# Kernel optimization log

Measured on AMD Instinct MI355X. Metric: run time of the kernel, lower is better.

Reference implementation:

```python
import jax, jax.numpy as jnp
import numpy as np

HIDDEN = 768
NUM_HEADS = 12
HEAD_DIM = HIDDEN // NUM_HEADS
B, S = 4, 2048


def setup_inputs() -> dict:
    key = jax.random.key(0)
    ks = jax.random.split(key, 10)
    scale = 1.0 / np.sqrt(HIDDEN)
    return {
        "hidden_states": jax.random.normal(ks[0], (B, S, HIDDEN), dtype=jnp.float32),
        "attention_mask": jnp.ones((B, S), dtype=jnp.float32),
        "Wq": jax.random.normal(ks[1], (HIDDEN, HIDDEN), dtype=jnp.float32) * scale,
        "bq": jnp.zeros((HIDDEN,), dtype=jnp.float32),
        "Wk": jax.random.normal(ks[2], (HIDDEN, HIDDEN), dtype=jnp.float32) * scale,
        "bk": jnp.zeros((HIDDEN,), dtype=jnp.float32),
        "Wv": jax.random.normal(ks[3], (HIDDEN, HIDDEN), dtype=jnp.float32) * scale,
        "bv": jnp.zeros((HIDDEN,), dtype=jnp.float32),
        "Wo": jax.random.normal(ks[4], (HIDDEN, HIDDEN), dtype=jnp.float32) * scale,
        "bo": jnp.zeros((HIDDEN,), dtype=jnp.float32),
    }


def reference(hidden_states, attention_mask, Wq, bq, Wk, bk, Wv, bv, Wo, bo):
    b, s, _ = hidden_states.shape
    # nn.Linear: x @ W.T + b  (W is [out, in])
    Q = hidden_states @ Wq.T + bq
    K = hidden_states @ Wk.T + bk
    V = hidden_states @ Wv.T + bv
    # [b, s, h*d] -> [b, h, s, d]
    Q = Q.reshape(b, s, NUM_HEADS, HEAD_DIM).transpose(0, 2, 1, 3)
    K = K.reshape(b, s, NUM_HEADS, HEAD_DIM).transpose(0, 2, 1, 3)
    V = V.reshape(b, s, NUM_HEADS, HEAD_DIM).transpose(0, 2, 1, 3)
    # scores: [b, h, s, s]
    scores = jnp.einsum("bhqd,bhkd->bhqk", Q, K) / jnp.sqrt(
        jnp.asarray(HEAD_DIM, dtype=Q.dtype))
    # mask: [b, s] -> additive bias broadcast over heads and query dim
    bias = (1.0 - attention_mask)[:, None, None, :] * -10000.0
    scores = scores + bias
    probs = jax.nn.softmax(scores, axis=-1)  # dropout p=0.0 -> identity
    context = jnp.einsum("bhqk,bhkd->bhqd", probs, V)
    context = context.transpose(0, 2, 1, 3).reshape(b, s, HIDDEN)
    return context @ Wo.T + bo
```

## Files before the change

kernel.cpp:

```cpp
#include <hip/hip_runtime.h>
#include <hip/hip_bf16.h>

#define SEQ   2048
#define NH    12
#define MTOK  8192

typedef __attribute__((ext_vector_type(8))) short short8;
typedef __attribute__((ext_vector_type(4))) short short4v;
typedef __attribute__((ext_vector_type(4))) float f32x4;
typedef __attribute__((ext_vector_type(16))) float f32x16;
typedef __attribute__((ext_vector_type(2))) unsigned uint2v;

__device__ inline short f2bf(float x) {
  __hip_bfloat16 h = __float2bfloat16(x);
  return *(short*)&h;
}

#define GLL(gp, lp) __builtin_amdgcn_global_load_lds( \
    (const __attribute__((address_space(1))) void*)(gp), \
    (__attribute__((address_space(3))) void*)(lp), 16, 0, 0)

#define GLL4(gp, lp) __builtin_amdgcn_global_load_lds( \
    (const __attribute__((address_space(1))) void*)(gp), \
    (__attribute__((address_space(3))) void*)(lp), 4, 0, 0)

#define MFMA(a, b, c) __builtin_amdgcn_mfma_f32_16x16x32_bf16(a, b, c, 0, 0, 0)

#if !defined(__HIP_DEVICE_COMPILE__)
#define MFMA32(a, b, c) (c)
#else
#define MFMA32(a, b, c) __builtin_amdgcn_mfma_f32_32x32x16_bf16(a, b, c, 0, 0, 0)
#endif

#if !defined(__HIP_DEVICE_COMPILE__)
#define EXP2(x) (x)
#elif __has_builtin(__builtin_amdgcn_exp2f)
#define EXP2(x) __builtin_amdgcn_exp2f(x)
#else
#define EXP2(x) __expf((x) * 0.6931471805599453f)
#endif

__device__ inline unsigned pack2bf(float a, float b) {
  unsigned ua = __float_as_uint(a) + 0x8000u;
  unsigned ub = __float_as_uint(b) + 0x8000u;
#if defined(__HIP_DEVICE_COMPILE__) && __has_builtin(__builtin_amdgcn_perm)
  return __builtin_amdgcn_perm(ub, ua, 0x07060302u);
#else
  return (ub & 0xFFFF0000u) | (ua >> 16);
#endif
}

__device__ inline unsigned packtrunc2(float a, float b) {
#if defined(__HIP_DEVICE_COMPILE__) && __has_builtin(__builtin_amdgcn_perm)
  return __builtin_amdgcn_perm(__float_as_uint(b), __float_as_uint(a),
                               0x07060302u);
#else
  return (__float_as_uint(b) & 0xFFFF0000u) | (__float_as_uint(a) >> 16);
#endif
}

__device__ inline uint2v lane32swap(unsigned a, unsigned b) {
#if defined(__HIP_DEVICE_COMPILE__) && __has_builtin(__builtin_amdgcn_permlane32_swap)
  return __builtin_amdgcn_permlane32_swap(a, b, false, false);
#else
  int lane = (int)(threadIdx.x & 63);
  unsigned xa = (unsigned)__shfl((int)a, lane ^ 32, 64);
  unsigned xb = (unsigned)__shfl((int)b, lane ^ 32, 64);
  bool hi = lane >= 32;
  uint2v r;
  r.x = hi ? xb : a;
  r.y = hi ? b : xa;
  return r;
#endif
}

union PackFrag {
  unsigned u[2];
  short4v s;
};

union Frag8 {
  unsigned u[4];
  short8 s;
};

#define QSCALE 0.18033688011112042f
#define MBSCALE -14426.950408889634f

__global__ __launch_bounds__(256) void prep(
    const float* __restrict__ hs, const float* __restrict__ Wq,
    const float* __restrict__ Wk, const float* __restrict__ Wv,
    const float* __restrict__ Wo, const float* __restrict__ mask,
    short* __restrict__ Xb, short* __restrict__ Wqkvb,
    short* __restrict__ Wob, float* __restrict__ mbias) {
  int bid = blockIdx.x;
  if (bid < 6144) {
    int i = bid * 256 + threadIdx.x;
    float4 v = ((const float4*)hs)[i];
    short4v o;
    o[0] = f2bf(v.x); o[1] = f2bf(v.y); o[2] = f2bf(v.z); o[3] = f2bf(v.w);
    ((short4v*)Xb)[i] = o;
  } else if (bid < 6144 + 2304) {
    int idx = (bid - 6144) * 256 + threadIdx.x;
    int r = idx / 192, c = (idx - r * 192) * 4;
    const float* src;
    short* dst;
    int rr;
    if (r < 768)       { src = Wq; rr = r;        dst = Wqkvb; }
    else if (r < 1536) { src = Wk; rr = r - 768;  dst = Wqkvb; }
    else if (r < 2304) { src = Wv; rr = r - 1536; dst = Wqkvb; }
    else               { src = Wo; rr = r - 2304; dst = Wob; r = rr; }
    float4 v = *(const float4*)&src[(size_t)rr * 768 + c];
    short4v o;
    o[0] = f2bf(v.x); o[1] = f2bf(v.y); o[2] = f2bf(v.z); o[3] = f2bf(v.w);
    *(short4v*)&dst[(size_t)r * 768 + c] = o;
  } else {
    int i = (bid - 6144 - 2304) * 256 + threadIdx.x;
    if (i < MTOK) mbias[i] = (1.f - mask[i]) * MBSCALE;
  }
}

#define GEMM_BK64_LOOP(Aptr, Bptr)                                            \
  __shared__ __align__(16) short As[128 * 64];                                \
  __shared__ __align__(16) short Bs[128 * 64];                                \
  const int t = threadIdx.x;                                                  \
  const int wid = t >> 6, lane = t & 63, l15 = lane & 15, quad = lane >> 4;   \
  const int bm = blockIdx.x * 128, bn = blockIdx.y * 128;                     \
  const int mq = (wid & 1) * 64, nq = (wid >> 1) * 64;                        \
  const int srow8 = lane >> 3;                                                \
  const int schunk = lane & 7;                                                \
  const int scol = (schunk ^ srow8) * 8;                                      \
  f32x4 acc[4][4] = {};                                                       \
  const short *gA[4], *gB[4];                                                 \
  _Pragma("unroll") for (int g = 0; g < 4; ++g) {                             \
    int row = wid * 32 + g * 8 + srow8;                                       \
    gA[g] = (Aptr) + (size_t)(bm + row) * 768 + scol;                         \
    gB[g] = (Bptr) + (size_t)(bn + row) * 768 + scol;                         \
  }                                                                           \
  for (int k0 = 0; k0 < 768; k0 += 64) {                                      \
    _Pragma("unroll") for (int g = 0; g < 4; ++g)                             \
      GLL(gA[g] + k0, &As[(wid * 32 + g * 8) * 64]);                          \
    _Pragma("unroll") for (int g = 0; g < 4; ++g)                             \
      GLL(gB[g] + k0, &Bs[(wid * 32 + g * 8) * 64]);                          \
    __syncthreads();                                                          \
    _Pragma("unroll") for (int ks = 0; ks < 2; ++ks) {                        \
      short8 a[4], b[4];                                                      \
      _Pragma("unroll") for (int mt = 0; mt < 4; ++mt)                        \
        a[mt] = *(const short8*)&As[(mq + mt * 16 + l15) * 64 +               \
                                    (((ks * 4 + quad) ^ (l15 & 7)) * 8)];     \
      _Pragma("unroll") for (int nt = 0; nt < 4; ++nt)                        \
        b[nt] = *(const short8*)&Bs[(nq + nt * 16 + l15) * 64 +               \
                                    (((ks * 4 + quad) ^ (l15 & 7)) * 8)];     \
      _Pragma("unroll") for (int mt = 0; mt < 4; ++mt)                        \
        _Pragma("unroll") for (int nt = 0; nt < 4; ++nt)                      \
          acc[mt][nt] = MFMA(a[mt], b[nt], acc[mt][nt]);                      \
    }                                                                         \
    __syncthreads();                                                          \
  }

__global__ __launch_bounds__(256) void gemm_qkv(
    const short* __restrict__ A, const short* __restrict__ B,
    const float* __restrict__ bq, const float* __restrict__ bk,
    const float* __restrict__ bv, short* __restrict__ Qb,
    short* __restrict__ Kb, short* __restrict__ Vt) {
  GEMM_BK64_LOOP(A, B)

  const int seg = bn >= 1536 ? 2 : (bn >= 768 ? 1 : 0);
  const float* bias = seg == 0 ? bq : (seg == 1 ? bk : bv);
  const int colbase = bn - seg * 768;

  if (seg < 2) {
    short* dst = seg == 0 ? Qb : Kb;
    const float sc = seg == 0 ? QSCALE : 1.f;
#pragma unroll
    for (int mt = 0; mt < 4; ++mt)
#pragma unroll
      for (int nt = 0; nt < 4; ++nt) {
        int col = colbase + nq + nt * 16 + l15;
        float bias_v = bias[col];
#pragma unroll
        for (int i = 0; i < 4; ++i) {
          int row = bm + mq + mt * 16 + quad * 4 + i;
          dst[(size_t)row * 768 + col] = f2bf((acc[mt][nt][i] + bias_v) * sc);
        }
      }
  } else {
#pragma unroll
    for (int mt = 0; mt < 4; ++mt) {
      int row0 = bm + mq + mt * 16 + quad * 4;
      int b_ = row0 >> 11, s = row0 & 2047;
#pragma unroll
      for (int nt = 0; nt < 4; ++nt) {
        int col = colbase + nq + nt * 16 + l15;
        float bias_v = bias[col];
        int h = col >> 6, d = col & 63;
        short4v pv;
#pragma unroll
        for (int i = 0; i < 4; ++i) pv[i] = f2bf(acc[mt][nt][i] + bias_v);
        *(short4v*)&Vt[(((size_t)b_ * NH + h) * 64 + d) * 2048 + s] = pv;
      }
    }
  }
}

__global__ __launch_bounds__(256) void gemm_out(
    const short* __restrict__ A, const short* __restrict__ B,
    const float* __restrict__ bias, float* __restrict__ C) {
  GEMM_BK64_LOOP(A, B)

#pragma unroll
  for (int mt = 0; mt < 4; ++mt)
#pragma unroll
    for (int nt = 0; nt < 4; ++nt) {
      int col = bn + nq + nt * 16 + l15;
      float bias_v = bias[col];
#pragma unroll
      for (int i = 0; i < 4; ++i) {
        int row = bm + mq + mt * 16 + quad * 4 + i;
        C[(size_t)row * 768 + col] = acc[mt][nt][i] + bias_v;
      }
    }
}

__global__ __launch_bounds__(256, 3) void attn_v13(
    const short* __restrict__ Qb, const short* __restrict__ Kb,
    const short* __restrict__ Vt, const float* __restrict__ maskb,
    short* __restrict__ Ctx) {
  __shared__ __align__(16) short Ks[3][64 * 64];
  __shared__ __align__(16) short Vs[3][64 * 64];
  __shared__ __align__(16) float Mbs[3][64];
  const int t = threadIdx.x;
  const int w = t >> 6, lane = t & 63, l31 = lane & 31, hi = lane >> 5;
  const int bh = blockIdx.x, b = bh / NH, h = bh % NH;
  const int q0 = blockIdx.y * 128;

  short8 qb[4];
  {
    int rowq = b * 2048 + q0 + w * 32 + l31;
    const short* qp = &Qb[(size_t)rowq * 768 + h * 64 + hi * 8];
#pragma unroll
    for (int kc = 0; kc < 4; ++kc) qb[kc] = *(const short8*)&qp[kc * 16];
  }

  f32x16 O0 = {}, O1 = {}, lacc = {};
  short8 ones8;
#pragma unroll
  for (int j = 0; j < 8; ++j) ones8[j] = (short)0x3F80;

  const int r0 = w * 16 + (lane >> 3);
  const int pc = lane & 7;
  const int swz0 = (pc ^ (r0 & 7)) * 8;
  const int swz1 = (pc ^ ((r0 + 8) & 7)) * 8;
  const short* gK0 = Kb + (size_t)(b * 2048 + r0) * 768 + h * 64 + swz0;
  const short* gK1 = Kb + (size_t)(b * 2048 + r0 + 8) * 768 + h * 64 + swz1;
  const short* gV0 = Vt + ((size_t)bh * 64 + r0) * 2048 + swz0;
  const short* gV1 = Vt + ((size_t)bh * 64 + r0 + 8) * 2048 + swz1;
  const float* gmb = maskb + b * 2048 + lane;
  const int rs = l31 & 7;

#define STAGE(tt, s) do {                                                     \
    const size_t kn = (size_t)(((tt) & 31) * 64);                             \
    GLL4(gmb + kn, &Mbs[s][0]);                                               \
    GLL(gK0 + kn * 768, &Ks[s][(w * 16) * 64]);                               \
    GLL(gK1 + kn * 768, &Ks[s][(w * 16 + 8) * 64]);                           \
    GLL(gV0 + kn, &Vs[s][(w * 16) * 64]);                                     \
    GLL(gV1 + kn, &Vs[s][(w * 16 + 8) * 64]);                                 \
  } while (0)

#define TILE_SYNC() do {                                                      \
    asm volatile("s_waitcnt vmcnt(5)" ::: "memory");                          \
    __builtin_amdgcn_s_barrier();                                             \
    __builtin_amdgcn_sched_barrier(0);                                        \
  } while (0)

  STAGE(0, 0);
  STAGE(1, 1);
  TILE_SYNC();

  int cur = 0;
  for (int ti = 0; ti < 32; ++ti) {
    const int nx2 = (cur == 0) ? 2 : cur - 1;
    STAGE(ti + 2, nx2);

    short8 pfrag[4];

#pragma unroll
    for (int kb2 = 0; kb2 < 2; ++kb2) {
      f32x16 S;
#pragma unroll
      for (int g = 0; g < 4; ++g) {
        f32x4 m4 = *(const f32x4*)&Mbs[cur][kb2 * 32 + g * 8 + hi * 4];
        S[4 * g + 0] = m4[0]; S[4 * g + 1] = m4[1];
        S[4 * g + 2] = m4[2]; S[4 * g + 3] = m4[3];
      }
#pragma unroll
      for (int kc = 0; kc < 4; ++kc) {
        short8 ka = *(const short8*)&Ks[cur][(kb2 * 32 + l31) * 64 +
                                            (((kc * 2 + hi) ^ rs) * 8)];
        S = MFMA32(ka, qb[kc], S);
      }
      unsigned pk[4][2];
#pragma unroll
      for (int g = 0; g < 4; ++g) {
        float p0 = EXP2(S[4 * g + 0]);
        float p1 = EXP2(S[4 * g + 1]);
        float p2 = EXP2(S[4 * g + 2]);
        float p3 = EXP2(S[4 * g + 3]);
        pk[g][0] = packtrunc2(p0, p1);
        pk[g][1] = packtrunc2(p2, p3);
      }
#pragma unroll
      for (int half = 0; half < 2; ++half) {
        Frag8 f;
        uint2v ra = lane32swap(pk[half * 2][0], pk[half * 2 + 1][0]);
        uint2v rb = lane32swap(pk[half * 2][1], pk[half * 2 + 1][1]);
        f.u[0] = ra.x;
        f.u[1] = rb.x;
        f.u[2] = ra.y;
        f.u[3] = rb.y;
        pfrag[kb2 * 2 + half] = f.s;
      }
    }

#pragma unroll
    for (int c = 0; c < 4; ++c) lacc = MFMA32(ones8, pfrag[c], lacc);

#pragma unroll
    for (int c = 0; c < 4; ++c) {
      short8 av0 = *(const short8*)&Vs[cur][(l31) * 64 +
                                           (((c * 2 + hi) ^ rs) * 8)];
      short8 av1 = *(const short8*)&Vs[cur][(32 + l31) * 64 +
                                           (((c * 2 + hi) ^ rs) * 8)];
      O0 = MFMA32(av0, pfrag[c], O0);
      O1 = MFMA32(av1, pfrag[c], O1);
    }

    TILE_SYNC();
    cur = (cur == 2) ? 0 : cur + 1;
  }

  {
    float inv = 1.f / lacc[0];
    int rowq = b * 2048 + q0 + w * 32 + l31;
    short* cp = &Ctx[(size_t)rowq * 768 + h * 64 + hi * 4];
#pragma unroll
    for (int g = 0; g < 4; ++g) {
      PackFrag pf0, pf1;
      pf0.u[0] = pack2bf(O0[4 * g + 0] * inv, O0[4 * g + 1] * inv);
      pf0.u[1] = pack2bf(O0[4 * g + 2] * inv, O0[4 * g + 3] * inv);
      *(short4v*)&cp[g * 8] = pf0.s;
      pf1.u[0] = pack2bf(O1[4 * g + 0] * inv, O1[4 * g + 1] * inv);
      pf1.u[1] = pack2bf(O1[4 * g + 2] * inv, O1[4 * g + 3] * inv);
      *(short4v*)&cp[32 + g * 8] = pf1.s;
    }
  }
#undef STAGE
#undef TILE_SYNC
}

extern "C" void kernel_launch(void* const* d_in, const int* in_sizes, int n_in,
                              void* d_out, int out_size, void* d_ws,
                              size_t ws_size, hipStream_t stream) {
  const float* hs   = (const float*)d_in[0];
  const float* mask = (const float*)d_in[1];
  const float* Wq   = (const float*)d_in[2];
  const float* bq   = (const float*)d_in[3];
  const float* Wk   = (const float*)d_in[4];
  const float* bk   = (const float*)d_in[5];
  const float* Wv   = (const float*)d_in[6];
  const float* bv   = (const float*)d_in[7];
  const float* Wo   = (const float*)d_in[8];
  const float* bo   = (const float*)d_in[9];

  char* ws = (char*)d_ws;
  short* Xb    = (short*)(ws);
  short* Wqkvb = (short*)(ws + 12582912);
  short* Wob   = (short*)(ws + 16121856);
  short* Qb    = (short*)(ws + 17301504);
  short* Kb    = (short*)(ws + 29884416);
  short* Vtg   = (short*)(ws + 42467328);
  short* Ctxb  = (short*)(ws + 55050240);
  float* mbias = (float*)(ws + 67633152);

  prep<<<8480, 256, 0, stream>>>(hs, Wq, Wk, Wv, Wo, mask,
                                 Xb, Wqkvb, Wob, mbias);
  gemm_qkv<<<dim3(64, 18), 256, 0, stream>>>(Xb, Wqkvb, bq, bk, bv,
                                             Qb, Kb, Vtg);
  attn_v13<<<dim3(48, 16), 256, 0, stream>>>(Qb, Kb, Vtg, mbias, Ctxb);
  gemm_out<<<dim3(64, 6), 256, 0, stream>>>(Ctxb, Wob, bo, (float*)d_out);
}
```

Baseline: 220.8 us.

## Pipeline GEMM K-loop with a three-stage LDS ring buffer

Replaces the single-buffered BK=64 GEMM loop (load, sync, compute, sync) with a BK=32 three-slot ring. Loads run two stages ahead, paced by an explicit vmcnt wait and one barrier per iteration, so global-to-LDS copies overlap the MFMA work. The XOR swizzle is adapted to 32-wide rows. The tail issues redundant wrapped loads (kk%24), which wastes some bandwidth, and correctness depends on the vmcnt counting being right.

```diff
diff --git a/kernel.cpp b/kernel.cpp
--- a/kernel.cpp
+++ b/kernel.cpp
@@ -120,50 +120,62 @@
   }
 }
 
-#define GEMM_BK64_LOOP(Aptr, Bptr)                                            \
-  __shared__ __align__(16) short As[128 * 64];                                \
-  __shared__ __align__(16) short Bs[128 * 64];                                \
+#define GEMM_BK32_RING(Aptr, Bptr)                                            \
+  __shared__ __align__(16) short As[3][128 * 32];                             \
+  __shared__ __align__(16) short Bs[3][128 * 32];                             \
   const int t = threadIdx.x;                                                  \
   const int wid = t >> 6, lane = t & 63, l15 = lane & 15, quad = lane >> 4;   \
   const int bm = blockIdx.x * 128, bn = blockIdx.y * 128;                     \
   const int mq = (wid & 1) * 64, nq = (wid >> 1) * 64;                        \
-  const int srow8 = lane >> 3;                                                \
-  const int schunk = lane & 7;                                                \
-  const int scol = (schunk ^ srow8) * 8;                                      \
+  const int srow = lane >> 2;                                                 \
+  const int schunk = lane & 3;                                                \
   f32x4 acc[4][4] = {};                                                       \
-  const short *gA[4], *gB[4];                                                 \
-  _Pragma("unroll") for (int g = 0; g < 4; ++g) {                             \
-    int row = wid * 32 + g * 8 + srow8;                                       \
+  const short *gA[2], *gB[2];                                                 \
+  _Pragma("unroll") for (int g = 0; g < 2; ++g) {                             \
+    int row = wid * 32 + g * 16 + srow;                                       \
+    int scol = (schunk ^ (row & 3)) * 8;                                      \
     gA[g] = (Aptr) + (size_t)(bm + row) * 768 + scol;                         \
     gB[g] = (Bptr) + (size_t)(bn + row) * 768 + scol;                         \
   }                                                                           \
-  for (int k0 = 0; k0 < 768; k0 += 64) {                                      \
-    _Pragma("unroll") for (int g = 0; g < 4; ++g)                             \
-      GLL(gA[g] + k0, &As[(wid * 32 + g * 8) * 64]);                          \
-    _Pragma("unroll") for (int g = 0; g < 4; ++g)                             \
-      GLL(gB[g] + k0, &Bs[(wid * 32 + g * 8) * 64]);                          \
-    __syncthreads();                                                          \
-    _Pragma("unroll") for (int ks = 0; ks < 2; ++ks) {                        \
-      short8 a[4], b[4];                                                      \
-      _Pragma("unroll") for (int mt = 0; mt < 4; ++mt)                        \
-        a[mt] = *(const short8*)&As[(mq + mt * 16 + l15) * 64 +               \
-                                    (((ks * 4 + quad) ^ (l15 & 7)) * 8)];     \
+  GSTAGE(0, 0);                                                               \
+  GSTAGE(1, 1);                                                               \
+  asm volatile("s_waitcnt vmcnt(4)" ::: "memory");                            \
+  __builtin_amdgcn_s_barrier();                                               \
+  __builtin_amdgcn_sched_barrier(0);                                          \
+  int cur = 0;                                                                \
+  for (int ti = 0; ti < 24; ++ti) {                                           \
+    const int nx2 = (cur == 0) ? 2 : cur - 1;                   \
+    GSTAGE(ti + 2, nx2);                                                      \
+    short8 a[4], b[4];                                                        \
+    _Pragma("unroll") for (int mt = 0; mt < 4; ++mt)                          \
+      a[mt] = *(const short8*)&As[cur][(mq + mt * 16 + l15) * 32 +            \
+                                       ((quad ^ (l15 & 3)) * 8)];             \
+    _Pragma("unroll") for (int nt = 0; nt < 4; ++nt)                          \
+      b[nt] = *(const short8*)&Bs[cur][(nq + nt * 16 + l15) * 32 +            \
+                                       ((quad ^ (l15 & 3)) * 8)];             \
+    _Pragma("unroll") for (int mt = 0; mt < 4; ++mt)                          \
       _Pragma("unroll") for (int nt = 0; nt < 4; ++nt)                        \
-        b[nt] = *(const short8*)&Bs[(nq + nt * 16 + l15) * 64 +               \
-                                    (((ks * 4 + quad) ^ (l15 & 7)) * 8)];     \
-      _Pragma("unroll") for (int mt = 0; mt < 4; ++mt)                        \
-        _Pragma("unroll") for (int nt = 0; nt < 4; ++nt)                      \
-          acc[mt][nt] = MFMA(a[mt], b[nt], acc[mt][nt]);                      \
+        acc[mt][nt] = MFMA(a[mt], b[nt], acc[mt][nt]);                        \
+    asm volatile("s_waitcnt vmcnt(4)" ::: "memory");                          \
+    __builtin_amdgcn_s_barrier();                                             \
+    __builtin_amdgcn_sched_barrier(0);                                        \
+    cur = (cur == 2) ? 0 : cur + 1;                                           \
+  }
+
+#define GSTAGE(kk, s) do {                                                    \
+    const int k0g = ((kk) % 24) * 32;                                         \
+    _Pragma("unroll") for (int g = 0; g < 2; ++g) {                           \
+      GLL(gA[g] + k0g, &As[s][(wid * 32 + g * 16) * 32]);                     \
+      GLL(gB[g] + k0g, &Bs[s][(wid * 32 + g * 16) * 32]);                     \
     }                                                                         \
-    __syncthreads();                                                          \
-  }
+  } while (0)
 
 __global__ __launch_bounds__(256) void gemm_qkv(
     const short* __restrict__ A, const short* __restrict__ B,
     const float* __restrict__ bq, const float* __restrict__ bk,
     const float* __restrict__ bv, short* __restrict__ Qb,
     short* __restrict__ Kb, short* __restrict__ Vt) {
-  GEMM_BK64_LOOP(A, B)
+  GEMM_BK32_RING(A, B)
 
   const int seg = bn >= 1536 ? 2 : (bn >= 768 ? 1 : 0);
   const float* bias = seg == 0 ? bq : (seg == 1 ? bk : bv);
@@ -206,7 +218,7 @@
 __global__ __launch_bounds__(256) void gemm_out(
     const short* __restrict__ A, const short* __restrict__ B,
     const float* __restrict__ bias, float* __restrict__ C) {
-  GEMM_BK64_LOOP(A, B)
+  GEMM_BK32_RING(A, B)
 
 #pragma unroll
   for (int mt = 0; mt < 4; ++mt)
```

New measurement: 239.9 us. 8.6% more time.

## Rewrite projection GEMMs as 8-wave 256x128 double-buffered ping-pong pipeline

Applied to the files above, without the earlier changes.

Replaces the single-buffered 128x128 GEMM loop with a 512-thread, 256x128 tile kernel that double-buffers A/B in LDS. The next k-slice is prefetched via global_load_lds while MFMAs run, using barrier and setprio interleaving between wave groups. This aims to hide global load latency and raise MFMA utilisation in the QKV and output projections. The larger LDS footprint (about 96 KB per block) may limit occupancy, and the grid shrinks to fewer blocks.

```diff
diff --git a/kernel.cpp b/kernel.cpp
--- a/kernel.cpp
+++ b/kernel.cpp
@@ -120,50 +120,76 @@
   }
 }
 
-#define GEMM_BK64_LOOP(Aptr, Bptr)                                            \
-  __shared__ __align__(16) short As[128 * 64];                                \
-  __shared__ __align__(16) short Bs[128 * 64];                                \
+#define GS8(kk, s) do {                                                       \
+    const int k0g = ((kk) % 12) * 64;                                         \
+    _Pragma("unroll") for (int g = 0; g < 4; ++g)                             \
+      GLL(gA[g] + k0g, &As[s][(wid * 32 + g * 8) * 64]);                      \
+    _Pragma("unroll") for (int g = 0; g < 2; ++g)                             \
+      GLL(gB[g] + k0g, &Bs[s][(wid * 16 + g * 8) * 64]);                      \
+  } while (0)
+
+#define GEMM_8P_CORE(Aptr, Bptr)                                              \
+  __shared__ __align__(16) short As[2][256 * 64];                             \
+  __shared__ __align__(16) short Bs[2][128 * 64];                             \
   const int t = threadIdx.x;                                                  \
   const int wid = t >> 6, lane = t & 63, l15 = lane & 15, quad = lane >> 4;   \
-  const int bm = blockIdx.x * 128, bn = blockIdx.y * 128;                     \
-  const int mq = (wid & 1) * 64, nq = (wid >> 1) * 64;                        \
-  const int srow8 = lane >> 3;                                                \
-  const int schunk = lane & 7;                                                \
+  const int bm = blockIdx.x * 256, bn = blockIdx.y * 128;                     \
+  const int wm = wid & 1, wn = wid >> 1;                                      \
+  const int srow8 = lane >> 3, schunk = lane & 7;                             \
   const int scol = (schunk ^ srow8) * 8;                                      \
-  f32x4 acc[4][4] = {};                                                       \
-  const short *gA[4], *gB[4];                                                 \
-  _Pragma("unroll") for (int g = 0; g < 4; ++g) {                             \
-    int row = wid * 32 + g * 8 + srow8;                                       \
-    gA[g] = (Aptr) + (size_t)(bm + row) * 768 + scol;                         \
-    gB[g] = (Bptr) + (size_t)(bn + row) * 768 + scol;                         \
-  }                                                                           \
-  for (int k0 = 0; k0 < 768; k0 += 64) {                                      \
-    _Pragma("unroll") for (int g = 0; g < 4; ++g)                             \
-      GLL(gA[g] + k0, &As[(wid * 32 + g * 8) * 64]);                          \
-    _Pragma("unroll") for (int g = 0; g < 4; ++g)                             \
-      GLL(gB[g] + k0, &Bs[(wid * 32 + g * 8) * 64]);                          \
-    __syncthreads();                                                          \
-    _Pragma("unroll") for (int ks = 0; ks < 2; ++ks) {                        \
-      short8 a[4], b[4];                                                      \
-      _Pragma("unroll") for (int mt = 0; mt < 4; ++mt)                        \
-        a[mt] = *(const short8*)&As[(mq + mt * 16 + l15) * 64 +               \
-                                    (((ks * 4 + quad) ^ (l15 & 7)) * 8)];     \
-      _Pragma("unroll") for (int nt = 0; nt < 4; ++nt)                        \
-        b[nt] = *(const short8*)&Bs[(nq + nt * 16 + l15) * 64 +               \
-                                    (((ks * 4 + quad) ^ (l15 & 7)) * 8)];     \
-      _Pragma("unroll") for (int mt = 0; mt < 4; ++mt)                        \
-        _Pragma("unroll") for (int nt = 0; nt < 4; ++nt)                      \
-          acc[mt][nt] = MFMA(a[mt], b[nt], acc[mt][nt]);                      \
+  f32x4 acc[8][2] = {};                                                       \
+  const short *gA[4], *gB[2];                                                 \
+  _Pragma("unroll") for (int g = 0; g < 4; ++g)                               \
+    gA[g] = (Aptr) + (size_t)(bm + wid * 32 + g * 8 + srow8) * 768 + scol;    \
+  _Pragma("unroll") for (int g = 0; g < 2; ++g)                               \
+    gB[g] = (Bptr) + (size_t)(bn + wid * 16 + g * 8 + srow8) * 768 + scol;    \
+  GS8(0, 0);                                                                  \
+  asm volatile("s_waitcnt vmcnt(0)" ::: "memory");                            \
+  __builtin_amdgcn_s_barrier();                                               \
+  __builtin_amdgcn_sched_barrier(0);                                          \
+  for (int ti = 0; ti < 12; ++ti) {                                           \
+    const int cur = ti & 1;                                                   \
+    if (ti) {                                                                 \
+      asm volatile("s_waitcnt vmcnt(0)" ::: "memory");                        \
+      __builtin_amdgcn_s_barrier();                                           \
+      __builtin_amdgcn_sched_barrier(0);                                      \
     }                                                                         \
-    __syncthreads();                                                          \
-  }
-
-__global__ __launch_bounds__(256) void gemm_qkv(
+    short8 bfr[2][2];                                                         \
+    _Pragma("unroll") for (int p = 0; p < 4; ++p) {                           \
+      short8 afr[2][2];                                                       \
+      _Pragma("unroll") for (int j = 0; j < 2; ++j)                           \
+        _Pragma("unroll") for (int ks = 0; ks < 2; ++ks)                      \
+          afr[j][ks] = *(const short8*)&As[cur][                              \
+              (wm * 128 + (p * 2 + j) * 16 + l15) * 64 +                      \
+              (((ks * 4 + quad) ^ (l15 & 7)) * 8)];                           \
+      if (p == 0) {                                                           \
+        _Pragma("unroll") for (int nt = 0; nt < 2; ++nt)                      \
+          _Pragma("unroll") for (int ks = 0; ks < 2; ++ks)                    \
+            bfr[nt][ks] = *(const short8*)&Bs[cur][                           \
+                (wn * 32 + nt * 16 + l15) * 64 +                              \
+                (((ks * 4 + quad) ^ (l15 & 7)) * 8)];                         \
+        GS8(ti + 1, cur ^ 1);                                                 \
+      }                                                                       \
+      __builtin_amdgcn_s_barrier();                                           \
+      __builtin_amdgcn_sched_barrier(0);                                      \
+      __builtin_amdgcn_s_setprio(1);                                          \
+      _Pragma("unroll") for (int ks = 0; ks < 2; ++ks)                        \
+        _Pragma("unroll") for (int j = 0; j < 2; ++j)                         \
+          _Pragma("unroll") for (int nt = 0; nt < 2; ++nt)                    \
+            acc[p * 2 + j][nt] =                                              \
+                MFMA(afr[j][ks], bfr[nt][ks], acc[p * 2 + j][nt]);            \
+      __builtin_amdgcn_s_setprio(0);                                          \
+      __builtin_amdgcn_s_barrier();                                           \
+      __builtin_amdgcn_sched_barrier(0);                                      \
+    }                                                                         \
+  }
+
+__global__ __launch_bounds__(512, 2) void gemm_qkv(
     const short* __restrict__ A, const short* __restrict__ B,
     const float* __restrict__ bq, const float* __restrict__ bk,
     const float* __restrict__ bv, short* __restrict__ Qb,
     short* __restrict__ Kb, short* __restrict__ Vt) {
-  GEMM_BK64_LOOP(A, B)
+  GEMM_8P_CORE(A, B)
 
   const int seg = bn >= 1536 ? 2 : (bn >= 768 ? 1 : 0);
   const float* bias = seg == 0 ? bq : (seg == 1 ? bk : bv);
@@ -173,25 +199,25 @@
     short* dst = seg == 0 ? Qb : Kb;
     const float sc = seg == 0 ? QSCALE : 1.f;
 #pragma unroll
-    for (int mt = 0; mt < 4; ++mt)
-#pragma unroll
-      for (int nt = 0; nt < 4; ++nt) {
-        int col = colbase + nq + nt * 16 + l15;
+    for (int mt = 0; mt < 8; ++mt)
+#pragma unroll
+      for (int nt = 0; nt < 2; ++nt) {
+        int col = colbase + wn * 32 + nt * 16 + l15;
         float bias_v = bias[col];
 #pragma unroll
         for (int i = 0; i < 4; ++i) {
-          int row = bm + mq + mt * 16 + quad * 4 + i;
+          int row = bm + wm * 128 + mt * 16 + quad * 4 + i;
           dst[(size_t)row * 768 + col] = f2bf((acc[mt][nt][i] + bias_v) * sc);
         }
       }
   } else {
 #pragma unroll
-    for (int mt = 0; mt < 4; ++mt) {
-      int row0 = bm + mq + mt * 16 + quad * 4;
+    for (int mt = 0; mt < 8; ++mt) {
+      int row0 = bm + wm * 128 + mt * 16 + quad * 4;
       int b_ = row0 >> 11, s = row0 & 2047;
 #pragma unroll
-      for (int nt = 0; nt < 4; ++nt) {
-        int col = colbase + nq + nt * 16 + l15;
+      for (int nt = 0; nt < 2; ++nt) {
+        int col = colbase + wn * 32 + nt * 16 + l15;
         float bias_v = bias[col];
         int h = col >> 6, d = col & 63;
         short4v pv;
@@ -203,20 +229,20 @@
   }
 }
 
-__global__ __launch_bounds__(256) void gemm_out(
+__global__ __launch_bounds__(512, 2) void gemm_out(
     const short* __restrict__ A, const short* __restrict__ B,
     const float* __restrict__ bias, float* __restrict__ C) {
-  GEMM_BK64_LOOP(A, B)
-
-#pragma unroll
-  for (int mt = 0; mt < 4; ++mt)
-#pragma unroll
-    for (int nt = 0; nt < 4; ++nt) {
-      int col = bn + nq + nt * 16 + l15;
+  GEMM_8P_CORE(A, B)
+
+#pragma unroll
+  for (int mt = 0; mt < 8; ++mt)
+#pragma unroll
+    for (int nt = 0; nt < 2; ++nt) {
+      int col = bn + wn * 32 + nt * 16 + l15;
       float bias_v = bias[col];
 #pragma unroll
       for (int i = 0; i < 4; ++i) {
-        int row = bm + mq + mt * 16 + quad * 4 + i;
+        int row = bm + wm * 128 + mt * 16 + quad * 4 + i;
         C[(size_t)row * 768 + col] = acc[mt][nt][i] + bias_v;
       }
     }
@@ -384,8 +410,8 @@
 
   prep<<<8480, 256, 0, stream>>>(hs, Wq, Wk, Wv, Wo, mask,
                                  Xb, Wqkvb, Wob, mbias);
-  gemm_qkv<<<dim3(64, 18), 256, 0, stream>>>(Xb, Wqkvb, bq, bk, bv,
+  gemm_qkv<<<dim3(32, 18), 512, 0, stream>>>(Xb, Wqkvb, bq, bk, bv,
                                              Qb, Kb, Vtg);
   attn_v13<<<dim3(48, 16), 256, 0, stream>>>(Qb, Kb, Vtg, mbias, Ctxb);
-  gemm_out<<<dim3(64, 6), 256, 0, stream>>>(Ctxb, Wob, bo, (float*)d_out);
-}
+  gemm_out<<<dim3(32, 6), 512, 0, stream>>>(Ctxb, Wob, bo, (float*)d_out);
+}
```

Result: slower. 242.0 us (+9.6%).
